# Performance work log

Hardware: AMD Instinct MI355X
Metric: run time of the kernel (lower is better)

Reference implementation:

```python
import jax, jax.numpy as jnp
import numpy as np


def setup_inputs() -> dict:
    key = jax.random.key(0)
    ks = jax.random.split(key, 8)
    B, M, N, F, H, O = 4, 4096, 4096, 8, 128, 8
    feat = jax.random.normal(ks[0], (B, N, F), dtype=jnp.float32)
    adj = jax.random.uniform(ks[1], (B, M, N), dtype=jnp.float32)
    # MLP params (Linear: y = x @ W.T + b), torch default-like scale
    def lin(k, fan_in, fan_out):
        lim = 1.0 / np.sqrt(fan_in)
        kw, kb = jax.random.split(k)
        W = jax.random.uniform(kw, (fan_out, fan_in), minval=-lim, maxval=lim, dtype=jnp.float32)
        b = jax.random.uniform(kb, (fan_out,), minval=-lim, maxval=lim, dtype=jnp.float32)
        return W, b
    W1, b1 = lin(ks[2], F, H)
    W2, b2 = lin(ks[3], H, H)
    W3, b3 = lin(ks[4], H, O)
    return {"feat": feat, "adj": adj, "W1": W1, "b1": b1, "W2": W2, "b2": b2, "W3": W3, "b3": b3}


def reference(feat, adj, W1, b1, W2, b2, W3, b3):
    # b = sum_n adj[..., m, n] * feat[..., n, f]  ==  adj @ feat
    b = jnp.einsum('bmn,bnf->bmf', adj, feat)  # [B, M, F]
    h = jax.nn.elu(b @ W1.T + b1)              # [B, M, H]
    h = jax.nn.elu(h @ W2.T + b2)              # [B, M, H]
    c = h @ W3.T + b3                          # [B, M, O]
    return c
```

## Files before the change

kernel.cpp:

```cpp
#include <hip/hip_runtime.h>
#include <cstdint>
#include <cstddef>

#define B_ 4
#define M_ 4096
#define N_ 4096
#define F_ 8
#define H_ 128
#define O_ 8

__device__ __forceinline__ uint32_t f2bf1(float x) {
    uint32_t u = __float_as_uint(x);
    return (u + 0x7fffu + ((u >> 16) & 1u)) >> 16;
}

__device__ __forceinline__ void bf8dec(uint4 w, float* f) {
    f[0] = __uint_as_float(w.x << 16);
    f[1] = __uint_as_float(w.x & 0xffff0000u);
    f[2] = __uint_as_float(w.y << 16);
    f[3] = __uint_as_float(w.y & 0xffff0000u);
    f[4] = __uint_as_float(w.z << 16);
    f[5] = __uint_as_float(w.z & 0xffff0000u);
    f[6] = __uint_as_float(w.w << 16);
    f[7] = __uint_as_float(w.w & 0xffff0000u);
}

__device__ __forceinline__ float elu(float x) {
    return x > 0.f ? x : (__expf(x) - 1.f);
}

__global__ __launch_bounds__(256, 2)
void k_adjfeat(const float* __restrict__ adj, const float* __restrict__ feat,
               float* __restrict__ bmat) {
    __shared__ uint4 sfeat[N_];

    const int tid = threadIdx.x;
    const int bb  = blockIdx.x >> 8;
    const int rb  = blockIdx.x & 255;

    const float4* fsrc = (const float4*)(feat + (size_t)bb * (N_ * F_));
    for (int n = tid; n < N_; n += 256) {
        float4 lo = fsrc[2 * n];
        float4 hi = fsrc[2 * n + 1];
        uint4 w;
        w.x = f2bf1(lo.x) | (f2bf1(lo.y) << 16);
        w.y = f2bf1(lo.z) | (f2bf1(lo.w) << 16);
        w.z = f2bf1(hi.x) | (f2bf1(hi.y) << 16);
        w.w = f2bf1(hi.z) | (f2bf1(hi.w) << 16);
        sfeat[(n & 3) * 1024 + (n >> 2)] = w;
    }
    __syncthreads();

    const int lane = tid & 63;
    const int wv   = tid >> 6;
    const int m0   = rb * 16 + wv * 4;

    const float4* arow = (const float4*)(adj + (size_t)(bb * M_ + m0) * N_);

    float acc[4][8];
#pragma unroll
    for (int r = 0; r < 4; ++r)
#pragma unroll
        for (int f = 0; f < 8; ++f) acc[r][f] = 0.f;

#pragma unroll 1
    for (int c = 0; c < 16; ++c) {
        const int ni = (c << 6) + lane;
        float4 a0 = arow[ni];
        float4 a1 = arow[ni + 1024];
        float4 a2 = arow[ni + 2048];
        float4 a3 = arow[ni + 3072];
        uint4 w0 = sfeat[ni];
        uint4 w1 = sfeat[1024 + ni];
        uint4 w2 = sfeat[2048 + ni];
        uint4 w3 = sfeat[3072 + ni];

        float av[4][4] = {{a0.x, a1.x, a2.x, a3.x},
                          {a0.y, a1.y, a2.y, a3.y},
                          {a0.z, a1.z, a2.z, a3.z},
                          {a0.w, a1.w, a2.w, a3.w}};
        uint4 ww[4] = {w0, w1, w2, w3};
#pragma unroll
        for (int k = 0; k < 4; ++k) {
            float f[8];
            bf8dec(ww[k], f);
#pragma unroll
            for (int r = 0; r < 4; ++r) {
                const float a = av[k][r];
#pragma unroll
                for (int j = 0; j < 8; ++j)
                    acc[r][j] = fmaf(a, f[j], acc[r][j]);
            }
        }
    }

#pragma unroll
    for (int r = 0; r < 4; ++r)
#pragma unroll
        for (int j = 0; j < 8; ++j) {
            float v = acc[r][j];
            v += __shfl_xor(v, 32, 64);
            v += __shfl_xor(v, 16, 64);
            v += __shfl_xor(v, 8, 64);
            v += __shfl_xor(v, 4, 64);
            v += __shfl_xor(v, 2, 64);
            v += __shfl_xor(v, 1, 64);
            acc[r][j] = v;
        }

    float my = 0.f;
#pragma unroll
    for (int r = 0; r < 4; ++r)
#pragma unroll
        for (int j = 0; j < 8; ++j)
            if (lane == r * 8 + j) my = acc[r][j];
    if (lane < 32)
        bmat[(size_t)(bb * M_ + m0 + (lane >> 3)) * 8 + (lane & 7)] = my;
}

__global__ __launch_bounds__(256, 2)
void k_mlp(const float* __restrict__ bmat,
           const float* __restrict__ W1, const float* __restrict__ b1,
           const float* __restrict__ W2, const float* __restrict__ b2,
           const float* __restrict__ W3, const float* __restrict__ b3,
           float* __restrict__ out) {
    __shared__ alignas(16) float sW1[H_ * F_];
    __shared__ float sB1[H_];
    __shared__ alignas(16) unsigned short sW2b[H_ * 136];
    __shared__ float sB2[H_];
    __shared__ alignas(16) float sW3[O_ * 132];
    __shared__ float sB3[O_];
    __shared__ alignas(16) float sB[32 * 8];
    __shared__ alignas(16) unsigned short sHb[32 * 136];

    const int tid = threadIdx.x;

    for (int i = tid; i < H_ * F_ / 4; i += 256)
        ((float4*)sW1)[i] = ((const float4*)W1)[i];

    for (int i8 = tid; i8 < H_ * H_ / 8; i8 += 256) {
        const int idx = i8 * 8;
        const int o = idx >> 7, k = idx & 127;
        const int oct = k >> 3;
        const int octs = (oct & 8) | ((oct + (o & 7)) & 7);
        float4 lo = ((const float4*)W2)[i8 * 2];
        float4 hi = ((const float4*)W2)[i8 * 2 + 1];
        uint4 w;
        w.x = f2bf1(lo.x) | (f2bf1(lo.y) << 16);
        w.y = f2bf1(lo.z) | (f2bf1(lo.w) << 16);
        w.z = f2bf1(hi.x) | (f2bf1(hi.y) << 16);
        w.w = f2bf1(hi.z) | (f2bf1(hi.w) << 16);
        *((uint4*)&sW2b[o * 136 + octs * 8]) = w;
    }

    for (int i = tid; i < O_ * H_ / 4; i += 256) {
        const int idx = i * 4;
        const int o = idx >> 7, k = idx & 127;
        *((float4*)&sW3[o * 132 + k]) = ((const float4*)W3)[i];
    }
    if (tid < H_) { sB1[tid] = b1[tid]; sB2[tid] = b2[tid]; }
    if (tid < O_) sB3[tid] = b3[tid];
    sB[tid] = bmat[(size_t)blockIdx.x * 256 + tid];
    __syncthreads();

    const int lane = tid & 63;
    const int wv   = tid >> 6;
    const int r0   = wv * 8;

    float w1a[8], w1b[8];
    {
        float4 x0 = *(const float4*)&sW1[lane * 8];
        float4 x1 = *(const float4*)&sW1[lane * 8 + 4];
        float4 y0 = *(const float4*)&sW1[(lane + 64) * 8];
        float4 y1 = *(const float4*)&sW1[(lane + 64) * 8 + 4];
        w1a[0]=x0.x; w1a[1]=x0.y; w1a[2]=x0.z; w1a[3]=x0.w;
        w1a[4]=x1.x; w1a[5]=x1.y; w1a[6]=x1.z; w1a[7]=x1.w;
        w1b[0]=y0.x; w1b[1]=y0.y; w1b[2]=y0.z; w1b[3]=y0.w;
        w1b[4]=y1.x; w1b[5]=y1.y; w1b[6]=y1.z; w1b[7]=y1.w;
    }
    const float bias1a = sB1[lane], bias1b = sB1[lane + 64];
#pragma unroll
    for (int r = 0; r < 8; ++r) {
        const float* bp = &sB[(r0 + r) * 8];
        float4 v0 = *(const float4*)bp;
        float4 v1 = *(const float4*)(bp + 4);
        float bv[8] = {v0.x, v0.y, v0.z, v0.w, v1.x, v1.y, v1.z, v1.w};
        float t0 = bias1a, t1 = bias1b;
#pragma unroll
        for (int j = 0; j < 8; ++j) {
            t0 = fmaf(bv[j], w1a[j], t0);
            t1 = fmaf(bv[j], w1b[j], t1);
        }
        sHb[(r0 + r) * 136 + lane]      = (unsigned short)f2bf1(elu(t0));
        sHb[(r0 + r) * 136 + lane + 64] = (unsigned short)f2bf1(elu(t1));
    }
    __syncthreads();

    float acc0[8], acc1[8];
#pragma unroll
    for (int r = 0; r < 8; ++r) { acc0[r] = 0.f; acc1[r] = 0.f; }
    const int swz = lane & 7;
#pragma unroll 1
    for (int oct = 0; oct < 16; ++oct) {
        const int col = ((oct & 8) | ((oct + swz) & 7)) << 3;
        uint4 wa = *(const uint4*)&sW2b[lane * 136 + col];
        uint4 wb = *(const uint4*)&sW2b[(lane + 64) * 136 + col];
        float A[8], Bv[8];
        bf8dec(wa, A);
        bf8dec(wb, Bv);
#pragma unroll
        for (int r = 0; r < 8; ++r) {
            uint4 hw = *(const uint4*)&sHb[(r0 + r) * 136 + (oct << 3)];
            float h[8];
            bf8dec(hw, h);
#pragma unroll
            for (int j = 0; j < 8; ++j) {
                acc0[r] = fmaf(h[j], A[j], acc0[r]);
                acc1[r] = fmaf(h[j], Bv[j], acc1[r]);
            }
        }
    }
    const float bias2a = sB2[lane], bias2b = sB2[lane + 64];
#pragma unroll
    for (int r = 0; r < 8; ++r) {
        sHb[(r0 + r) * 136 + lane]      = (unsigned short)f2bf1(elu(acc0[r] + bias2a));
        sHb[(r0 + r) * 136 + lane + 64] = (unsigned short)f2bf1(elu(acc1[r] + bias2b));
    }
    __syncthreads();

    const int rr  = lane >> 3;
    const int oo  = lane & 7;
    const int row = r0 + rr;
    float s = 0.f;
#pragma unroll
    for (int oct = 0; oct < 16; ++oct) {
        uint4 hw = *(const uint4*)&sHb[row * 136 + (oct << 3)];
        float h[8];
        bf8dec(hw, h);
        const float* wp = &sW3[oo * 132 + (oct << 3)];
        float4 g0 = *(const float4*)wp;
        float4 g1 = *(const float4*)(wp + 4);
        float g[8] = {g0.x, g0.y, g0.z, g0.w, g1.x, g1.y, g1.z, g1.w};
#pragma unroll
        for (int j = 0; j < 8; ++j) s = fmaf(h[j], g[j], s);
    }
    s += sB3[oo];
    out[(size_t)(blockIdx.x * 32 + row) * 8 + oo] = s;
}

extern "C" void kernel_launch(void* const* d_in, const int* in_sizes, int n_in,
                              void* d_out, int out_size, void* d_ws, size_t ws_size,
                              hipStream_t stream) {
    const float* feat = (const float*)d_in[0];
    const float* adj  = (const float*)d_in[1];
    const float* W1   = (const float*)d_in[2];
    const float* b1   = (const float*)d_in[3];
    const float* W2   = (const float*)d_in[4];
    const float* b2   = (const float*)d_in[5];
    const float* W3   = (const float*)d_in[6];
    const float* b3   = (const float*)d_in[7];
    float* bmat = (float*)d_ws;
    float* outp = (float*)d_out;

    k_adjfeat<<<dim3(B_ * 256), dim3(256), 0, stream>>>(adj, feat, bmat);
    k_mlp<<<dim3(512), dim3(256), 0, stream>>>(bmat, W1, b1, W2, b2, W3, b3, outp);
}
```

Measured before the change: 399.0 us.

## Fuse adjacency aggregation and MLP into a single kernel

Merges the adj@feat reduction kernel and the three-layer MLP kernel into one launch. Each block reuses a shared-memory region for the bf16 feature cache and then for the MLP weights and fp32 hidden activations. The intermediate matrix no longer goes through global memory, and one kernel launch is removed. In exchange, every block of the larger grid reloads and converts W2 and the other weights, the hidden activations are kept in fp32 without the bank swizzle, and the blocks keep holding shared memory while doing the MLP work.

```diff
diff --git a/kernel.cpp b/kernel.cpp
--- a/kernel.cpp
+++ b/kernel.cpp
@@ -30,9 +30,20 @@
 }
 
 __global__ __launch_bounds__(256, 2)
-void k_adjfeat(const float* __restrict__ adj, const float* __restrict__ feat,
-               float* __restrict__ bmat) {
-    __shared__ uint4 sfeat[N_];
+void k_fused(const float* __restrict__ adj, const float* __restrict__ feat,
+             const float* __restrict__ W1, const float* __restrict__ b1,
+             const float* __restrict__ W2, const float* __restrict__ b2,
+             const float* __restrict__ W3, const float* __restrict__ b3,
+             float* __restrict__ out) {
+    __shared__ alignas(16) unsigned char smem[65536];
+    uint4* sfeat = (uint4*)smem;
+    float* sW1 = (float*)smem;
+    float* sW3 = (float*)(smem + 4096);
+    float* sB1 = (float*)(smem + 8320);
+    float* sB2 = (float*)(smem + 8832);
+    float* sB3 = (float*)(smem + 9344);
+    float* sH  = (float*)(smem + 9376);
+    unsigned short* sW2b = (unsigned short*)(smem + 17824);
 
     const int tid = threadIdx.x;
     const int bb  = blockIdx.x >> 8;
@@ -108,32 +119,7 @@
             acc[r][j] = v;
         }
 
-    float my = 0.f;
-#pragma unroll
-    for (int r = 0; r < 4; ++r)
-#pragma unroll
-        for (int j = 0; j < 8; ++j)
-            if (lane == r * 8 + j) my = acc[r][j];
-    if (lane < 32)
-        bmat[(size_t)(bb * M_ + m0 + (lane >> 3)) * 8 + (lane & 7)] = my;
-}
-
-__global__ __launch_bounds__(256, 2)
-void k_mlp(const float* __restrict__ bmat,
-           const float* __restrict__ W1, const float* __restrict__ b1,
-           const float* __restrict__ W2, const float* __restrict__ b2,
-           const float* __restrict__ W3, const float* __restrict__ b3,
-           float* __restrict__ out) {
-    __shared__ alignas(16) float sW1[H_ * F_];
-    __shared__ float sB1[H_];
-    __shared__ alignas(16) unsigned short sW2b[H_ * 136];
-    __shared__ float sB2[H_];
-    __shared__ alignas(16) float sW3[O_ * 132];
-    __shared__ float sB3[O_];
-    __shared__ alignas(16) float sB[32 * 8];
-    __shared__ alignas(16) unsigned short sHb[32 * 136];
-
-    const int tid = threadIdx.x;
+    __syncthreads();
 
     for (int i = tid; i < H_ * F_ / 4; i += 256)
         ((float4*)sW1)[i] = ((const float4*)W1)[i];
@@ -141,8 +127,6 @@
     for (int i8 = tid; i8 < H_ * H_ / 8; i8 += 256) {
         const int idx = i8 * 8;
         const int o = idx >> 7, k = idx & 127;
-        const int oct = k >> 3;
-        const int octs = (oct & 8) | ((oct + (o & 7)) & 7);
         float4 lo = ((const float4*)W2)[i8 * 2];
         float4 hi = ((const float4*)W2)[i8 * 2 + 1];
         uint4 w;
@@ -150,7 +134,7 @@
         w.y = f2bf1(lo.z) | (f2bf1(lo.w) << 16);
         w.z = f2bf1(hi.x) | (f2bf1(hi.y) << 16);
         w.w = f2bf1(hi.z) | (f2bf1(hi.w) << 16);
-        *((uint4*)&sW2b[o * 136 + octs * 8]) = w;
+        *((uint4*)&sW2b[o * 136 + k]) = w;
     }
 
     for (int i = tid; i < O_ * H_ / 4; i += 256) {
@@ -160,12 +144,7 @@
     }
     if (tid < H_) { sB1[tid] = b1[tid]; sB2[tid] = b2[tid]; }
     if (tid < O_) sB3[tid] = b3[tid];
-    sB[tid] = bmat[(size_t)blockIdx.x * 256 + tid];
     __syncthreads();
-
-    const int lane = tid & 63;
-    const int wv   = tid >> 6;
-    const int r0   = wv * 8;
 
     float w1a[8], w1b[8];
     {
@@ -180,72 +159,61 @@
     }
     const float bias1a = sB1[lane], bias1b = sB1[lane + 64];
 #pragma unroll
-    for (int r = 0; r < 8; ++r) {
-        const float* bp = &sB[(r0 + r) * 8];
-        float4 v0 = *(const float4*)bp;
-        float4 v1 = *(const float4*)(bp + 4);
-        float bv[8] = {v0.x, v0.y, v0.z, v0.w, v1.x, v1.y, v1.z, v1.w};
+    for (int r = 0; r < 4; ++r) {
         float t0 = bias1a, t1 = bias1b;
 #pragma unroll
         for (int j = 0; j < 8; ++j) {
-            t0 = fmaf(bv[j], w1a[j], t0);
-            t1 = fmaf(bv[j], w1b[j], t1);
-        }
-        sHb[(r0 + r) * 136 + lane]      = (unsigned short)f2bf1(elu(t0));
-        sHb[(r0 + r) * 136 + lane + 64] = (unsigned short)f2bf1(elu(t1));
-    }
-    __syncthreads();
-
-    float acc0[8], acc1[8];
-#pragma unroll
-    for (int r = 0; r < 8; ++r) { acc0[r] = 0.f; acc1[r] = 0.f; }
-    const int swz = lane & 7;
+            t0 = fmaf(acc[r][j], w1a[j], t0);
+            t1 = fmaf(acc[r][j], w1b[j], t1);
+        }
+        sH[(wv * 4 + r) * 132 + lane]      = elu(t0);
+        sH[(wv * 4 + r) * 132 + lane + 64] = elu(t1);
+    }
+
+    float a20[4], a21[4];
+#pragma unroll
+    for (int r = 0; r < 4; ++r) { a20[r] = 0.f; a21[r] = 0.f; }
 #pragma unroll 1
     for (int oct = 0; oct < 16; ++oct) {
-        const int col = ((oct & 8) | ((oct + swz) & 7)) << 3;
-        uint4 wa = *(const uint4*)&sW2b[lane * 136 + col];
-        uint4 wb = *(const uint4*)&sW2b[(lane + 64) * 136 + col];
+        uint4 wa = *(const uint4*)&sW2b[lane * 136 + (oct << 3)];
+        uint4 wb = *(const uint4*)&sW2b[(lane + 64) * 136 + (oct << 3)];
         float A[8], Bv[8];
         bf8dec(wa, A);
         bf8dec(wb, Bv);
 #pragma unroll
-        for (int r = 0; r < 8; ++r) {
-            uint4 hw = *(const uint4*)&sHb[(r0 + r) * 136 + (oct << 3)];
-            float h[8];
-            bf8dec(hw, h);
+        for (int r = 0; r < 4; ++r) {
+            const float* hp = &sH[(wv * 4 + r) * 132 + (oct << 3)];
+            float4 h0 = *(const float4*)hp;
+            float4 h1v = *(const float4*)(hp + 4);
+            float hv[8] = {h0.x, h0.y, h0.z, h0.w, h1v.x, h1v.y, h1v.z, h1v.w};
 #pragma unroll
             for (int j = 0; j < 8; ++j) {
-                acc0[r] = fmaf(h[j], A[j], acc0[r]);
-                acc1[r] = fmaf(h[j], Bv[j], acc1[r]);
+                a20[r] = fmaf(hv[j], A[j], a20[r]);
+                a21[r] = fmaf(hv[j], Bv[j], a21[r]);
             }
         }
     }
     const float bias2a = sB2[lane], bias2b = sB2[lane + 64];
 #pragma unroll
-    for (int r = 0; r < 8; ++r) {
-        sHb[(r0 + r) * 136 + lane]      = (unsigned short)f2bf1(elu(acc0[r] + bias2a));
-        sHb[(r0 + r) * 136 + lane + 64] = (unsigned short)f2bf1(elu(acc1[r] + bias2b));
-    }
-    __syncthreads();
-
-    const int rr  = lane >> 3;
-    const int oo  = lane & 7;
-    const int row = r0 + rr;
-    float s = 0.f;
-#pragma unroll
-    for (int oct = 0; oct < 16; ++oct) {
-        uint4 hw = *(const uint4*)&sHb[row * 136 + (oct << 3)];
-        float h[8];
-        bf8dec(hw, h);
-        const float* wp = &sW3[oo * 132 + (oct << 3)];
-        float4 g0 = *(const float4*)wp;
-        float4 g1 = *(const float4*)(wp + 4);
-        float g[8] = {g0.x, g0.y, g0.z, g0.w, g1.x, g1.y, g1.z, g1.w};
-#pragma unroll
-        for (int j = 0; j < 8; ++j) s = fmaf(h[j], g[j], s);
-    }
-    s += sB3[oo];
-    out[(size_t)(blockIdx.x * 32 + row) * 8 + oo] = s;
+    for (int r = 0; r < 4; ++r) {
+        sH[(wv * 4 + r) * 132 + lane]      = elu(a20[r] + bias2a);
+        sH[(wv * 4 + r) * 132 + lane + 64] = elu(a21[r] + bias2b);
+    }
+
+    if (lane < 32) {
+        const int rr = lane >> 3;
+        const int oo = lane & 7;
+        const float* hp = &sH[(wv * 4 + rr) * 132];
+        const float* wp = &sW3[oo * 132];
+        float s = sB3[oo];
+#pragma unroll
+        for (int k = 0; k < 128; k += 4) {
+            float4 h = *(const float4*)(hp + k);
+            float4 g = *(const float4*)(wp + k);
+            s = fmaf(h.x, g.x, fmaf(h.y, g.y, fmaf(h.z, g.z, fmaf(h.w, g.w, s))));
+        }
+        out[(size_t)(bb * M_ + m0 + rr) * 8 + oo] = s;
+    }
 }
 
 extern "C" void kernel_launch(void* const* d_in, const int* in_sizes, int n_in,
@@ -259,9 +227,8 @@
     const float* b2   = (const float*)d_in[5];
     const float* W3   = (const float*)d_in[6];
     const float* b3   = (const float*)d_in[7];
-    float* bmat = (float*)d_ws;
     float* outp = (float*)d_out;
 
-    k_adjfeat<<<dim3(B_ * 256), dim3(256), 0, stream>>>(adj, feat, bmat);
-    k_mlp<<<dim3(512), dim3(256), 0, stream>>>(bmat, W1, b1, W2, b2, W3, b3, outp);
-}
+    k_fused<<<dim3(B_ * 256), dim3(256), 0, stream>>>(
+        adj, feat, W1, b1, W2, b2, W3, b3, outp);
+}
```

New measurement: 396.3 us. No clear change (-0.7%).
